# Kernel optimization log

Measured on AMD Instinct MI355X. Metric: run time of the kernel, lower is better.

## Reference

```python
import jax, jax.numpy as jnp
import numpy as np

HIDDEN = 64
N_LAYERS = 3
WORLD_W = 1.0
WORLD_H = 1.0

silu = jax.nn.silu


def _lin(x, w, b):
    return x @ w + b


def setup_inputs() -> dict:
    key = jax.random.key(0)
    ks = jax.random.split(key, 32)
    B, N, H, L = 2, 512, HIDDEN, N_LAYERS
    s = 0.05
    inp = {
        "state": jax.random.uniform(ks[0], (B, N, 4), dtype=jnp.float32),
        "h_init_w": jax.random.normal(ks[1], (1, H), dtype=jnp.float32) * s,
        "h_init_b": jnp.zeros((H,), jnp.float32),
        # per-layer stacked params (L, ...)
        "edge_w1": jax.random.normal(ks[2], (L, 2 * H + 4, H), jnp.float32) * s,
        "edge_b1": jnp.zeros((L, H), jnp.float32),
        "edge_w2": jax.random.normal(ks[3], (L, H, H), jnp.float32) * s,
        "edge_b2": jnp.zeros((L, H), jnp.float32),
        "force_w1": jax.random.normal(ks[4], (L, H, H), jnp.float32) * s,
        "force_b1": jnp.zeros((L, H), jnp.float32),
        "force_w2": jax.random.normal(ks[5], (L, H, 1), jnp.float32) * s,
        "force_b2": jnp.zeros((L, 1), jnp.float32),
        "node_w1": jax.random.normal(ks[6], (L, 2 * H, H), jnp.float32) * s,
        "node_b1": jnp.zeros((L, H), jnp.float32),
        "node_w2": jax.random.normal(ks[7], (L, H, H), jnp.float32) * s,
        "node_b2": jnp.zeros((L, H), jnp.float32),
        "wall_w1": jax.random.normal(ks[8], (H + 4, H), jnp.float32) * s,
        "wall_b1": jnp.zeros((H,), jnp.float32),
        "wall_w2": jax.random.normal(ks[9], (H, H), jnp.float32) * s,
        "wall_b2": jnp.zeros((H,), jnp.float32),
        "wall_w3": jax.random.normal(ks[10], (H, 4), jnp.float32) * s,
        "wall_b3": jnp.zeros((4,), jnp.float32),
    }
    return inp


def _layer(h, pos, vel, ew1, eb1, ew2, eb2, fw1, fb1, fw2, fb2, nw1, nb1, nw2, nb2):
    B, N, H = h.shape
    # rel_pos[b,i,j] = pos[b,j] - pos[b,i]
    rel_pos = pos[:, None, :, :] - pos[:, :, None, :]          # (B,N,N,2)
    dist_sq = jnp.sum(rel_pos ** 2, axis=-1, keepdims=True)    # (B,N,N,1)
    dist = jnp.sqrt(dist_sq + 1e-8)
    normal = rel_pos / dist
    speed_sq = jnp.sum(vel ** 2, axis=-1, keepdims=True)       # (B,N,1)
    rel_vel = vel[:, None, :, :] - vel[:, :, None, :]
    approach = jnp.sum(rel_vel * normal, axis=-1, keepdims=True)
    h_i = jnp.broadcast_to(h[:, :, None, :], (B, N, N, H))
    h_j = jnp.broadcast_to(h[:, None, :, :], (B, N, N, H))
    sp_i = jnp.broadcast_to(speed_sq[:, :, None, :], (B, N, N, 1))
    sp_j = jnp.broadcast_to(speed_sq[:, None, :, :], (B, N, N, 1))
    edge_feat = jnp.concatenate([h_i, h_j, dist_sq, sp_i, sp_j, approach], axis=-1)
    m_ij = silu(_lin(silu(_lin(edge_feat, ew1, eb1)), ew2, eb2))  # (B,N,N,H)
    force_weight = _lin(silu(_lin(m_ij, fw1, fb1)), fw2, fb2)     # (B,N,N,1)
    mask = (1.0 - jnp.eye(N, dtype=h.dtype))[None, :, :, None]
    force = jnp.sum(force_weight * normal * mask, axis=2)         # (B,N,2)
    m_agg = jnp.sum(m_ij * mask, axis=2)                          # (B,N,H)
    h_new = _lin(silu(_lin(jnp.concatenate([h, m_agg], axis=-1), nw1, nb1)), nw2, nb2)
    return h_new, force


def reference(state, h_init_w, h_init_b, edge_w1, edge_b1, edge_w2, edge_b2,
              force_w1, force_b1, force_w2, force_b2,
              node_w1, node_b1, node_w2, node_b2,
              wall_w1, wall_b1, wall_w2, wall_b2, wall_w3, wall_b3):
    pos = state[:, :, :2]
    vel = state[:, :, 2:]
    speed = jnp.sqrt(jnp.sum(vel ** 2, axis=-1, keepdims=True))
    h = silu(_lin(speed, h_init_w, h_init_b))
    total_force = jnp.zeros_like(pos)
    for l in range(edge_w1.shape[0]):
        h, f = _layer(h, pos, vel,
                      edge_w1[l], edge_b1[l], edge_w2[l], edge_b2[l],
                      force_w1[l], force_b1[l], force_w2[l], force_b2[l],
                      node_w1[l], node_b1[l], node_w2[l], node_b2[l])
        total_force = total_force + f
    wall_dists = jnp.stack([pos[:, :, 0], WORLD_W - pos[:, :, 0],
                            pos[:, :, 1], WORLD_H - pos[:, :, 1]], axis=-1)
    x = jnp.concatenate([h, wall_dists], axis=-1)
    wall_mag = _lin(silu(_lin(silu(_lin(x, wall_w1, wall_b1)), wall_w2, wall_b2)), wall_w3, wall_b3)  # (B,N,4)
    wall_normals = jnp.array([[1.0, 0.0], [-1.0, 0.0], [0.0, 1.0], [0.0, -1.0]], dtype=state.dtype)
    wall_force = jnp.einsum('bnw,wd->bnd', wall_mag, wall_normals)
    return total_force + wall_force
```

## Files before the change

kernel.cpp:

```cpp
#include <hip/hip_runtime.h>
#include <math.h>

#define H 64
#define NN 512
#define NB 2
#define NL 3
#define NBLK (NN * NB)

typedef _Float16 half8  __attribute__((ext_vector_type(8)));
typedef __fp16   fp16x2 __attribute__((ext_vector_type(2)));
typedef float    float4v __attribute__((ext_vector_type(4)));

union FragU { half8 h; unsigned int u[4]; uint4 q4; };
union F8    { float4 v4[2]; float f[8]; };

__device__ __forceinline__ float silu_f(float x) {
    float e = __expf(-x);
    return x * __builtin_amdgcn_rcpf(1.0f + e);
}

__device__ __forceinline__ unsigned int pk2(float a, float b) {
    fp16x2 h = __builtin_amdgcn_cvt_pkrtz(a, b);
    return __builtin_bit_cast(unsigned int, h);
}

__global__ __launch_bounds__(256) void k_setup(
    const float* __restrict__ state, const float* __restrict__ hiw,
    const float* __restrict__ hib, const float* __restrict__ ew1,
    const float* __restrict__ eb1, const float* __restrict__ ew2,
    const float* __restrict__ fw1, float* __restrict__ h,
    float* __restrict__ P, float* __restrict__ Q, float* __restrict__ faccum,
    uint4* __restrict__ wpack)
{
    const int bn  = blockIdx.x;
    const int tid = threadIdx.x;
    const int wv  = tid >> 6;
    const int lane = tid & 63;

    __shared__ float sh[64];
    __shared__ float sRed[4][64];
    __shared__ float sRedQ[4][64];

    if (tid < 64) {
        const float* st = state + bn * 4;
        float vx = st[2], vy = st[3];
        float s2 = vx * vx + vy * vy;
        if (tid < 2) faccum[bn * 2 + tid] = 0.0f;
        float hv = silu_f(sqrtf(s2) * hiw[tid] + hib[tid]);
        h[(size_t)bn * H + tid] = hv;
        sh[tid] = hv;
    }
    if (bn < 6) {
        const int pl = bn >> 1, mat = bn & 1;
        const float* src = (mat ? fw1 : ew2) + (size_t)pl * 4096;
        uint4* dst = wpack + ((size_t)pl * 2 + mat) * 512;
        for (int g = tid; g < 512; g += 256) {
            int f = g >> 6, ln = g & 63;
            int mt = f >> 1, kt = f & 1, qq = ln >> 4, mm = ln & 15;
            int cm  = mt * 16 + mm;
            int cin = kt * 32 + qq * 8;
            uint4 u;
            u.x = pk2(src[(cin + 0) * 64 + cm], src[(cin + 1) * 64 + cm]);
            u.y = pk2(src[(cin + 2) * 64 + cm], src[(cin + 3) * 64 + cm]);
            u.z = pk2(src[(cin + 4) * 64 + cm], src[(cin + 5) * 64 + cm]);
            u.w = pk2(src[(cin + 6) * 64 + cm], src[(cin + 7) * 64 + cm]);
            dst[g] = u;
        }
    }
    __syncthreads();

    {
        float pp = 0.0f, qp = 0.0f;
        const float* wp = ew1 + (size_t)(wv * 16) * 64 + lane;
        const float* wq = ew1 + (size_t)(64 + wv * 16) * 64 + lane;
#pragma unroll 8
        for (int k = 0; k < 16; k++) {
            float hk = sh[wv * 16 + k];
            pp += hk * wp[(size_t)k * 64];
            qp += hk * wq[(size_t)k * 64];
        }
        sRed[wv][lane]  = pp;
        sRedQ[wv][lane] = qp;
    }
    __syncthreads();
    if (wv == 0) {
        const float* st = state + bn * 4;
        float vx = st[2], vy = st[3];
        float s2 = vx * vx + vy * vy;
        P[(size_t)bn * 64 + lane] = eb1[lane] + sRed[0][lane] + sRed[1][lane]
                                  + sRed[2][lane] + sRed[3][lane];
        Q[(size_t)bn * 64 + lane] = sRedQ[0][lane] + sRedQ[1][lane]
                                  + sRedQ[2][lane] + sRedQ[3][lane]
                                  + s2 * ew1[130 * 64 + lane];
    }
}

__global__ __launch_bounds__(256, 2) void k_edge(
    const float* __restrict__ state,
    const float* __restrict__ P, const float* __restrict__ Q,
    float* __restrict__ Pout, float* __restrict__ Qout,
    const float* __restrict__ ew1_l,
    const uint4* __restrict__ wpackL,
    const float* __restrict__ eb2_l,
    const float* __restrict__ fb1_l,
    const float* __restrict__ fw2_l, const float* __restrict__ fb2_l,
    float* __restrict__ h, float* __restrict__ faccum,
    const float* __restrict__ nw1_l, const float* __restrict__ nb1_l,
    const float* __restrict__ nw2_l, const float* __restrict__ nb2_l,
    const float* __restrict__ ew1_n, const float* __restrict__ eb1_n,
    const float* __restrict__ ww1, const float* __restrict__ wb1,
    const float* __restrict__ ww2, const float* __restrict__ wb2,
    const float* __restrict__ ww3, const float* __restrict__ wb3,
    float* __restrict__ out, int last)
{
    const int i    = blockIdx.x;
    const int b    = blockIdx.y;
    const int tid  = threadIdx.x;
    const int wv   = tid >> 6;
    const int lane = tid & 63;
    const int q    = lane >> 4;
    const int m    = lane & 15;
    const int bn_i = b * NN + i;

    __shared__ float sW[128];
    __shared__ float sBias[192];
    __shared__ float sPB[64];
    __shared__ __align__(16) unsigned short sMT[4][16 * 72];
    __shared__ float sRed[4][64];
    __shared__ float sRedQ[4][64];
    __shared__ float sF[4][2];

    if (tid < 128) sW[tid] = ew1_l[(128 + (tid >> 6) * 3) * 64 + (tid & 63)];
    if (tid < 192) sBias[tid] = (tid < 64) ? eb2_l[tid]
                              : (tid < 128) ? fb1_l[tid - 64]
                              : fw2_l[tid - 128];

    FragU wreg[8], freg[8];
#pragma unroll
    for (int f = 0; f < 8; f++) {
        wreg[f].q4 = wpackL[f * 64 + lane];
        freg[f].q4 = wpackL[512 + f * 64 + lane];
    }

    const float4 sti = *(const float4*)&state[(size_t)bn_i * 4];
    const float  spi = sti.z * sti.z + sti.w * sti.w;
    if (tid < 64) sPB[tid] = P[(size_t)bn_i * 64 + tid] + spi * ew1_l[129 * 64 + tid];
    __syncthreads();

    const float fb2q = fb2_l[0] * 0.25f;

    F8 w0r[2], w3r[2], pbr[2];
    float4 b2r[4], fb1r[4], fw2r[4];
#pragma unroll
    for (int kt = 0; kt < 2; kt++) {
        const int c0 = kt * 32 + q * 8;
        w0r[kt].v4[0] = *(const float4*)&sW[c0];
        w0r[kt].v4[1] = *(const float4*)&sW[c0 + 4];
        w3r[kt].v4[0] = *(const float4*)&sW[64 + c0];
        w3r[kt].v4[1] = *(const float4*)&sW[64 + c0 + 4];
        pbr[kt].v4[0] = *(const float4*)&sPB[c0];
        pbr[kt].v4[1] = *(const float4*)&sPB[c0 + 4];
    }
#pragma unroll
    for (int mt = 0; mt < 4; mt++) {
        b2r[mt]  = *(const float4*)&sBias[mt * 16 + q * 4];
        fb1r[mt] = *(const float4*)&sBias[64 + mt * 16 + q * 4];
        fw2r[mt] = *(const float4*)&sBias[128 + mt * 16 + q * 4];
    }

    float maccp[16];
#pragma unroll
    for (int t = 0; t < 16; t++) maccp[t] = 0.0f;
    float fax = 0.0f, fay = 0.0f;

    unsigned short* MT = sMT[wv];

#pragma unroll 1
    for (int ck = 0; ck < 8; ck++) {
        const int jg = wv * 128 + ck * 16 + m;
        const float msk = (jg != i) ? 1.0f : 0.0f;

        float jnx, jny;
        FragU xb[2];
        {
            const float4 stj = *(const float4*)&state[(size_t)(b * NN + jg) * 4];
            float dx = stj.x - sti.x, dy = stj.y - sti.y;
            float ds = dx * dx + dy * dy;
            float rs = __builtin_amdgcn_rsqf(ds + 1e-8f);
            jnx = dx * rs;
            jny = dy * rs;
            float jap = (stj.z - sti.z) * jnx + (stj.w - sti.w) * jny;

#pragma unroll
            for (int kt = 0; kt < 2; kt++) {
                const int c0 = kt * 32 + q * 8;
                const float* Qr = &Q[(size_t)(b * NN + jg) * 64 + c0];
                F8 qv;
                qv.v4[0] = *(const float4*)Qr;
                qv.v4[1] = *(const float4*)(Qr + 4);
                float xv[8];
#pragma unroll
                for (int d = 0; d < 8; d++) {
                    float pre = pbr[kt].f[d] + qv.f[d] + ds * w0r[kt].f[d]
                              + jap * w3r[kt].f[d];
                    xv[d] = silu_f(pre);
                }
#pragma unroll
                for (int d = 0; d < 4; d++)
                    xb[kt].u[d] = pk2(xv[2 * d], xv[2 * d + 1]);
            }
        }

#pragma unroll
        for (int hf = 0; hf < 2; hf++) {
            float4v acc[2];
#pragma unroll
            for (int mt2 = 0; mt2 < 2; mt2++) {
                const float4 b2v = b2r[hf * 2 + mt2];
                acc[mt2][0] = b2v.x; acc[mt2][1] = b2v.y;
                acc[mt2][2] = b2v.z; acc[mt2][3] = b2v.w;
            }
#pragma unroll
            for (int kt = 0; kt < 2; kt++) {
#pragma unroll
                for (int mt2 = 0; mt2 < 2; mt2++) {
                    acc[mt2] = __builtin_amdgcn_mfma_f32_16x16x32_f16(
                        wreg[(hf * 2 + mt2) * 2 + kt].h, xb[kt].h, acc[mt2], 0, 0, 0);
                }
            }
#pragma unroll
            for (int mt2 = 0; mt2 < 2; mt2++) {
                const int mt = hf * 2 + mt2;
                float4v a = acc[mt2];
                float m0 = silu_f(a[0]);
                float m1 = silu_f(a[1]);
                float m2 = silu_f(a[2]);
                float m3 = silu_f(a[3]);
                maccp[mt * 4 + 0] = fmaf(m0, msk, maccp[mt * 4 + 0]);
                maccp[mt * 4 + 1] = fmaf(m1, msk, maccp[mt * 4 + 1]);
                maccp[mt * 4 + 2] = fmaf(m2, msk, maccp[mt * 4 + 2]);
                maccp[mt * 4 + 3] = fmaf(m3, msk, maccp[mt * 4 + 3]);
                uint2 dw = make_uint2(pk2(m0, m1), pk2(m2, m3));
                *(uint2*)&MT[m * 72 + mt * 16 + q * 4] = dw;
            }
        }

        float fdp = 0.0f;
        FragU xb2[2];
#pragma unroll
        for (int kt = 0; kt < 2; kt++)
            xb2[kt].q4 = *(uint4*)&MT[m * 72 + kt * 32 + q * 8];
#pragma unroll
        for (int hf = 0; hf < 2; hf++) {
            float4v acc2[2];
#pragma unroll
            for (int mt2 = 0; mt2 < 2; mt2++) {
                const float4 fb1v = fb1r[hf * 2 + mt2];
                acc2[mt2][0] = fb1v.x; acc2[mt2][1] = fb1v.y;
                acc2[mt2][2] = fb1v.z; acc2[mt2][3] = fb1v.w;
            }
#pragma unroll
            for (int kt = 0; kt < 2; kt++) {
#pragma unroll
                for (int mt2 = 0; mt2 < 2; mt2++) {
                    acc2[mt2] = __builtin_amdgcn_mfma_f32_16x16x32_f16(
                        freg[(hf * 2 + mt2) * 2 + kt].h, xb2[kt].h, acc2[mt2], 0, 0, 0);
                }
            }
#pragma unroll
            for (int mt2 = 0; mt2 < 2; mt2++) {
                const float4 fw2v = fw2r[hf * 2 + mt2];
                float4v a = acc2[mt2];
                fdp += silu_f(a[0]) * fw2v.x
                     + silu_f(a[1]) * fw2v.y
                     + silu_f(a[2]) * fw2v.z
                     + silu_f(a[3]) * fw2v.w;
            }
        }

        {
            float fd = fdp + fb2q;
            fax += fd * jnx;
            fay += fd * jny;
        }
    }

#pragma unroll
    for (int t = 0; t < 16; t++) {
        float v = maccp[t];
        v += __shfl_xor(v, 1, 64);
        v += __shfl_xor(v, 2, 64);
        v += __shfl_xor(v, 4, 64);
        v += __shfl_xor(v, 8, 64);
        maccp[t] = v;
    }
    if (m == 0) {
#pragma unroll
        for (int mt = 0; mt < 4; mt++)
#pragma unroll
          for (int r = 0; r < 4; r++)
            sRed[wv][mt * 16 + q * 4 + r] = maccp[mt * 4 + r];
    }
#pragma unroll
    for (int off = 1; off < 64; off <<= 1) {
        fax += __shfl_xor(fax, off, 64);
        fay += __shfl_xor(fay, off, 64);
    }
    if (lane == 0) {
        sF[wv][0] = fax;
        sF[wv][1] = fay;
    }
    __syncthreads();

    float* scr = (float*)sMT;
    const int c = lane;
    if (wv == 0) {
        float magg = sRed[0][c] + sRed[1][c] + sRed[2][c] + sRed[3][c];
        scr[c]      = h[(size_t)bn_i * 64 + c];
        scr[64 + c] = magg;
    }
    __syncthreads();

    {
        float part = 0.0f;
        const float* w = nw1_l + (size_t)(wv * 32) * 64 + c;
#pragma unroll 8
        for (int k = 0; k < 32; k++) part += scr[wv * 32 + k] * w[(size_t)k * 64];
        sRed[wv][c] = part;
    }
    __syncthreads();
    if (wv == 0) {
        float t1 = nb1_l[c] + sRed[0][c] + sRed[1][c] + sRed[2][c] + sRed[3][c];
        scr[128 + c] = silu_f(t1);
    }
    __syncthreads();

    {
        float part = 0.0f;
        const float* w = nw2_l + (size_t)(wv * 16) * 64 + c;
#pragma unroll 8
        for (int k = 0; k < 16; k++) part += scr[128 + wv * 16 + k] * w[(size_t)k * 64];
        sRed[wv][c] = part;
    }
    __syncthreads();

    if (wv == 0) {
        float hn  = nb2_l[c] + sRed[0][c] + sRed[1][c] + sRed[2][c] + sRed[3][c];
        scr[192 + c] = hn;
        if (!last) {
            h[(size_t)bn_i * 64 + c] = hn;
            float fxl = sF[0][0] + sF[1][0] + sF[2][0] + sF[3][0];
            float fyl = sF[0][1] + sF[1][1] + sF[2][1] + sF[3][1];
            if (c == 0) {
                faccum[bn_i * 2 + 0] += fxl;
                faccum[bn_i * 2 + 1] += fyl;
            }
        }
    }
    __syncthreads();

    if (!last) {
        float pp = 0.0f, qp = 0.0f;
        const float* wp = ew1_n + (size_t)(wv * 16) * 64 + c;
        const float* wq = ew1_n + (size_t)(64 + wv * 16) * 64 + c;
#pragma unroll 8
        for (int k = 0; k < 16; k++) {
            float hk = scr[192 + wv * 16 + k];
            pp += hk * wp[(size_t)k * 64];
            qp += hk * wq[(size_t)k * 64];
        }
        sRed[wv][c]  = pp;
        sRedQ[wv][c] = qp;
        __syncthreads();
        if (wv == 0) {
            Pout[(size_t)bn_i * 64 + c] = eb1_n[c] + sRed[0][c] + sRed[1][c]
                                        + sRed[2][c] + sRed[3][c];
            Qout[(size_t)bn_i * 64 + c] = sRedQ[0][c] + sRedQ[1][c]
                                        + sRedQ[2][c] + sRedQ[3][c]
                                        + spi * ew1_n[130 * 64 + c];
        }
        return;
    }

    if (wv != 0) return;

    if (c < 4) {
        float px = sti.x, py = sti.y;
        float wd = (c == 0) ? px : (c == 1) ? 1.0f - px : (c == 2) ? py : 1.0f - py;
        scr[256 + c] = wd;
    }
    float t2 = wb1[c];
#pragma unroll 4
    for (int k = 0; k < 64; k++) t2 += scr[192 + k] * ww1[k * 64 + c];
#pragma unroll
    for (int k = 0; k < 4; k++)  t2 += scr[256 + k] * ww1[(64 + k) * 64 + c];
    t2 = silu_f(t2);
    scr[320 + c] = t2;
    float u = wb2[c];
#pragma unroll 8
    for (int k = 0; k < 64; k++) u += scr[320 + k] * ww2[k * 64 + c];
    u = silu_f(u);
    scr[384 + c] = u;
    if (c < 4) {
        float mg = wb3[c];
        for (int k = 0; k < 64; k++) mg += scr[384 + k] * ww3[k * 4 + c];
        scr[448 + c] = mg;
    }
    if (c == 0) {
        float fxl = sF[0][0] + sF[1][0] + sF[2][0] + sF[3][0];
        float fyl = sF[0][1] + sF[1][1] + sF[2][1] + sF[3][1];
        float fx = faccum[bn_i * 2 + 0] + fxl + (scr[448 + 0] - scr[448 + 1]);
        float fy = faccum[bn_i * 2 + 1] + fyl + (scr[448 + 2] - scr[448 + 3]);
        out[bn_i * 2 + 0] = fx;
        out[bn_i * 2 + 1] = fy;
    }
}

extern "C" void kernel_launch(void* const* d_in, const int* in_sizes, int n_in,
                              void* d_out, int out_size, void* d_ws, size_t ws_size,
                              hipStream_t stream)
{
    const float* state = (const float*)d_in[0];
    const float* hiw   = (const float*)d_in[1];
    const float* hib   = (const float*)d_in[2];
    const float* ew1   = (const float*)d_in[3];
    const float* eb1   = (const float*)d_in[4];
    const float* ew2   = (const float*)d_in[5];
    const float* eb2   = (const float*)d_in[6];
    const float* fw1   = (const float*)d_in[7];
    const float* fb1   = (const float*)d_in[8];
    const float* fw2   = (const float*)d_in[9];
    const float* fb2   = (const float*)d_in[10];
    const float* nw1   = (const float*)d_in[11];
    const float* nb1   = (const float*)d_in[12];
    const float* nw2   = (const float*)d_in[13];
    const float* nb2   = (const float*)d_in[14];
    const float* ww1   = (const float*)d_in[15];
    const float* wb1   = (const float*)d_in[16];
    const float* ww2   = (const float*)d_in[17];
    const float* wb2   = (const float*)d_in[18];
    const float* ww3   = (const float*)d_in[19];
    const float* wb3   = (const float*)d_in[20];
    float* out = (float*)d_out;

    float* ws     = (float*)d_ws;
    float* h      = ws;
    float* P0     = h      + (size_t)NB * NN * H;
    float* Q0     = P0     + (size_t)NB * NN * H;
    float* P1     = Q0     + (size_t)NB * NN * H;
    float* Q1     = P1     + (size_t)NB * NN * H;
    float* faccum = Q1     + (size_t)NB * NN * H;
    float* wpackf = faccum + (size_t)NB * NN * 2;
    uint4* wpack  = (uint4*)(((uintptr_t)wpackf + 15) & ~(uintptr_t)15);

    float* Pb[2] = { P0, P1 };
    float* Qb[2] = { Q0, Q1 };

    k_setup<<<NBLK, 256, 0, stream>>>(state, hiw, hib, ew1, eb1,
                                      ew2, fw1, h, P0, Q0, faccum, wpack);

    for (int l = 0; l < NL; l++) {
        const int last = (l == NL - 1) ? 1 : 0;
        const int nl = last ? 0 : (l + 1);
        const int cur = l & 1, nxt = (l + 1) & 1;
        k_edge<<<dim3(NN, NB), 256, 0, stream>>>(
            state, Pb[cur], Qb[cur], Pb[nxt], Qb[nxt],
            ew1 + (size_t)l * 132 * 64,
            wpack + (size_t)l * 1024,
            eb2 + (size_t)l * 64,
            fb1 + (size_t)l * 64,
            fw2 + (size_t)l * 64, fb2 + (size_t)l,
            h, faccum,
            nw1 + (size_t)l * 128 * 64, nb1 + (size_t)l * 64,
            nw2 + (size_t)l * 64 * 64,  nb2 + (size_t)l * 64,
            ew1 + (size_t)nl * 132 * 64, eb1 + (size_t)nl * 64,
            ww1, wb1, ww2, wb2, ww3, wb3,
            out, last);
    }
}
```

Before: 231.5 us.

## Move force-MLP weight fragments and biases from registers to shared memory

The force-layer MFMA weight fragments are staged in shared memory instead of being held in 32 VGPRs per lane. The bias and fw2 vectors are now reloaded from LDS inside the edge loop instead of being kept in registers. An opaque zero offset stops the compiler from hoisting these loads back into registers. The min-blocks hint on launch_bounds is dropped, which aims to cut register pressure and spilling, possibly raising occupancy, at the cost of extra LDS traffic per iteration.

```diff
diff --git a/kernel.cpp b/kernel.cpp
--- a/kernel.cpp
+++ b/kernel.cpp
@@ -95,7 +95,7 @@
     }
 }
 
-__global__ __launch_bounds__(256, 2) void k_edge(
+__global__ __launch_bounds__(256) void k_edge(
     const float* __restrict__ state,
     const float* __restrict__ P, const float* __restrict__ Q,
     float* __restrict__ Pout, float* __restrict__ Qout,
@@ -126,6 +126,7 @@
     __shared__ float sBias[192];
     __shared__ float sPB[64];
     __shared__ __align__(16) unsigned short sMT[4][16 * 72];
+    __shared__ uint4 sFreg[512];
     __shared__ float sRed[4][64];
     __shared__ float sRedQ[4][64];
     __shared__ float sF[4][2];
@@ -135,12 +136,11 @@
                               : (tid < 128) ? fb1_l[tid - 64]
                               : fw2_l[tid - 128];
 
-    FragU wreg[8], freg[8];
-#pragma unroll
-    for (int f = 0; f < 8; f++) {
-        wreg[f].q4 = wpackL[f * 64 + lane];
-        freg[f].q4 = wpackL[512 + f * 64 + lane];
-    }
+    FragU wreg[8];
+#pragma unroll
+    for (int f = 0; f < 8; f++) wreg[f].q4 = wpackL[f * 64 + lane];
+    sFreg[tid]       = wpackL[512 + tid];
+    sFreg[256 + tid] = wpackL[512 + 256 + tid];
 
     const float4 sti = *(const float4*)&state[(size_t)bn_i * 4];
     const float  spi = sti.z * sti.z + sti.w * sti.w;
@@ -150,7 +150,6 @@
     const float fb2q = fb2_l[0] * 0.25f;
 
     F8 w0r[2], w3r[2], pbr[2];
-    float4 b2r[4], fb1r[4], fw2r[4];
 #pragma unroll
     for (int kt = 0; kt < 2; kt++) {
         const int c0 = kt * 32 + q * 8;
@@ -161,12 +160,6 @@
         pbr[kt].v4[0] = *(const float4*)&sPB[c0];
         pbr[kt].v4[1] = *(const float4*)&sPB[c0 + 4];
     }
-#pragma unroll
-    for (int mt = 0; mt < 4; mt++) {
-        b2r[mt]  = *(const float4*)&sBias[mt * 16 + q * 4];
-        fb1r[mt] = *(const float4*)&sBias[64 + mt * 16 + q * 4];
-        fw2r[mt] = *(const float4*)&sBias[128 + mt * 16 + q * 4];
-    }
 
     float maccp[16];
 #pragma unroll
@@ -177,6 +170,10 @@
 
 #pragma unroll 1
     for (int ck = 0; ck < 8; ck++) {
+        unsigned swoff = 0;
+        asm volatile("" : "+v"(swoff));
+        __builtin_assume((swoff & 3u) == 0);
+
         const int jg = wv * 128 + ck * 16 + m;
         const float msk = (jg != i) ? 1.0f : 0.0f;
 
@@ -216,7 +213,7 @@
             float4v acc[2];
 #pragma unroll
             for (int mt2 = 0; mt2 < 2; mt2++) {
-                const float4 b2v = b2r[hf * 2 + mt2];
+                const float4 b2v = *(const float4*)&sBias[swoff + (hf * 2 + mt2) * 16 + q * 4];
                 acc[mt2][0] = b2v.x; acc[mt2][1] = b2v.y;
                 acc[mt2][2] = b2v.z; acc[mt2][3] = b2v.w;
             }
@@ -255,7 +252,7 @@
             float4v acc2[2];
 #pragma unroll
             for (int mt2 = 0; mt2 < 2; mt2++) {
-                const float4 fb1v = fb1r[hf * 2 + mt2];
+                const float4 fb1v = *(const float4*)&sBias[swoff + 64 + (hf * 2 + mt2) * 16 + q * 4];
                 acc2[mt2][0] = fb1v.x; acc2[mt2][1] = fb1v.y;
                 acc2[mt2][2] = fb1v.z; acc2[mt2][3] = fb1v.w;
             }
@@ -263,13 +260,15 @@
             for (int kt = 0; kt < 2; kt++) {
 #pragma unroll
                 for (int mt2 = 0; mt2 < 2; mt2++) {
+                    FragU fr;
+                    fr.q4 = sFreg[swoff + ((hf * 2 + mt2) * 2 + kt) * 64 + lane];
                     acc2[mt2] = __builtin_amdgcn_mfma_f32_16x16x32_f16(
-                        freg[(hf * 2 + mt2) * 2 + kt].h, xb2[kt].h, acc2[mt2], 0, 0, 0);
+                        fr.h, xb2[kt].h, acc2[mt2], 0, 0, 0);
                 }
             }
 #pragma unroll
             for (int mt2 = 0; mt2 < 2; mt2++) {
-                const float4 fw2v = fw2r[hf * 2 + mt2];
+                const float4 fw2v = *(const float4*)&sBias[swoff + 128 + (hf * 2 + mt2) * 16 + q * 4];
                 float4v a = acc2[mt2];
                 fdp += silu_f(a[0]) * fw2v.x
                      + silu_f(a[1]) * fw2v.y
```

Result: no change. 236.1 us (+2.0%).
